# Kernel optimization log

Hardware: AMD Instinct MI355X
Metric: run time of the kernel (lower is better)

Reference implementation:

```python
import jax, jax.numpy as jnp
import numpy as np

HEAD = 64

PARAM_NAMES = ['x_r','x_w','x_k','x_v','x_a','x_g','w0','w1','w2','a0','a1','a2',
               'v0','v1','v2','g1','g2','k_k','k_a','r_k','W_r','W_k','W_v','W_o',
               'ln_x_w','ln_x_b','ln1_w','ln1_b','ln2_w','ln2_b','c_x_k','W_ck','W_cv']


def token_shift(x):
    # previous token, zero-padded at t=0 (stateless shift state)
    return jnp.pad(x, ((0, 0), (1, 0), (0, 0)))[:, :-1]


def layer_norm(x, w, b, eps=1e-5):
    m = jnp.mean(x, -1, keepdims=True)
    v = jnp.mean(jnp.square(x - m), -1, keepdims=True)
    return (x - m) * jax.lax.rsqrt(v + eps) * w + b


def group_norm_heads(x, w, b, H, eps=64e-5):
    # GroupNorm(H, C) as used by RWKV7 ln_x (eps = head_size * 1e-5)
    B, T, C = x.shape
    xh = x.reshape(B, T, H, C // H)
    m = jnp.mean(xh, -1, keepdims=True)
    v = jnp.mean(jnp.square(xh - m), -1, keepdims=True)
    xh = (xh - m) * jax.lax.rsqrt(v + eps)
    return xh.reshape(B, T, C) * w + b


def wkv7(r, w, k, v, a, b):
    # r,w,k,v,a,b: [B,T,H,N]; w is per-channel decay in (0,1)
    # S_t = S_{t-1} * diag(w_t) + (S_{t-1} @ a_t) b_t^T + v_t k_t^T ; y_t = S_t @ r_t
    B, T, H, N = r.shape
    def step(S, inp):
        r_t, w_t, k_t, v_t, a_t, b_t = inp
        sa = jnp.einsum('bhij,bhj->bhi', S, a_t)
        S = S * w_t[:, :, None, :] + sa[..., None] * b_t[:, :, None, :] + v_t[..., None] * k_t[:, :, None, :]
        y = jnp.einsum('bhij,bhj->bhi', S, r_t)
        return S, y
    xs = tuple(jnp.moveaxis(t, 1, 0) for t in (r, w, k, v, a, b))
    S0 = jnp.zeros((B, H, N, N), r.dtype)
    _, ys = jax.lax.scan(step, S0, xs)
    return jnp.moveaxis(ys, 0, 1)


def time_mix(x, v_first, p, is_first_layer):
    B, T, C = x.shape
    H, N = C // HEAD, HEAD
    xx = token_shift(x) - x
    xr = x + xx * p['x_r']; xw = x + xx * p['x_w']; xk = x + xx * p['x_k']
    xv = x + xx * p['x_v']; xa = x + xx * p['x_a']; xg = x + xx * p['x_g']
    r = xr @ p['W_r']
    w = -jax.nn.softplus(-(p['w0'] + jnp.tanh(xw @ p['w1']) @ p['w2'])) - 0.5
    k = xk @ p['W_k']
    v = xv @ p['W_v']
    if is_first_layer:
        v_first = v
    else:
        v = v + (v_first - v) * jax.nn.sigmoid(p['v0'] + (xv @ p['v1']) @ p['v2'])
    a = jax.nn.sigmoid(p['a0'] + (xa @ p['a1']) @ p['a2'])  # in-context learning rate
    g = jax.nn.sigmoid(xg @ p['g1']) @ p['g2']
    kk = (k * p['k_k']).reshape(B, T, H, N)
    kk = kk / jnp.maximum(jnp.linalg.norm(kk, axis=-1, keepdims=True), 1e-12)
    k = k * (1.0 + (a - 1.0) * p['k_a'])
    decay = jnp.exp(-jnp.exp(w)).reshape(B, T, H, N)
    rh = r.reshape(B, T, H, N)
    kh = k.reshape(B, T, H, N)
    vh = v.reshape(B, T, H, N)
    ah = a.reshape(B, T, H, N)
    y = wkv7(rh, decay, kh, vh, -kk, kk * ah).reshape(B, T, C)
    y = group_norm_heads(y, p['ln_x_w'], p['ln_x_b'], H)
    bonus = jnp.sum(rh * kh * p['r_k'], -1, keepdims=True) * vh
    y = y + bonus.reshape(B, T, C)
    return (y * g) @ p['W_o'], v_first


def channel_mix(x, p):
    xx = token_shift(x) - x
    k = x + xx * p['c_x_k']
    k = jnp.square(jax.nn.relu(k @ p['W_ck']))
    return k @ p['W_cv']


def encoder_forward(x, params):
    L = params['W_r'].shape[0]
    v_first = None
    for i in range(L):
        p = {n: params[n][i] for n in PARAM_NAMES}
        att, v_first = time_mix(layer_norm(x, p['ln1_w'], p['ln1_b']), v_first, p, i == 0)
        x = x + att
        x = x + channel_mix(layer_norm(x, p['ln2_w'], p['ln2_b']), p)
    return x


def setup_inputs() -> dict:
    key = jax.random.key(0)
    L, B, T, C = 6, 2, 512, 768
    H, N = C // HEAD, HEAD
    Dw, Da, Dv, Dg, F = 64, 64, 32, 128, 4 * C
    keys = iter(jax.random.split(key, 48))
    def rn(shape, s):
        return jax.random.normal(next(keys), shape, jnp.float32) * s
    def ru(shape):
        return jax.random.uniform(next(keys), shape, jnp.float32)
    inp = {
        'x': rn((B, T, C), 1.0),
        'x_r': ru((L, C)), 'x_w': ru((L, C)), 'x_k': ru((L, C)),
        'x_v': ru((L, C)), 'x_a': ru((L, C)), 'x_g': ru((L, C)),
        'w0': rn((L, C), 0.3), 'w1': rn((L, C, Dw), 0.02), 'w2': rn((L, Dw, C), 0.02),
        'a0': rn((L, C), 0.1), 'a1': rn((L, C, Da), 0.02), 'a2': rn((L, Da, C), 0.02),
        'v0': rn((L, C), 0.1), 'v1': rn((L, C, Dv), 0.02), 'v2': rn((L, Dv, C), 0.02),
        'g1': rn((L, C, Dg), 0.02), 'g2': rn((L, Dg, C), 0.02),
        'k_k': 0.85 + rn((L, C), 0.05), 'k_a': 1.0 + rn((L, C), 0.05),
        'r_k': rn((L, H, N), 0.1),
        'W_r': rn((L, C, C), 0.02), 'W_k': rn((L, C, C), 0.02),
        'W_v': rn((L, C, C), 0.02), 'W_o': rn((L, C, C), 0.02),
        'ln_x_w': 1.0 + rn((L, C), 0.05), 'ln_x_b': rn((L, C), 0.05),
        'ln1_w': 1.0 + rn((L, C), 0.05), 'ln1_b': rn((L, C), 0.05),
        'ln2_w': 1.0 + rn((L, C), 0.05), 'ln2_b': rn((L, C), 0.05),
        'c_x_k': ru((L, C)),
        'W_ck': rn((L, C, F), 0.02), 'W_cv': rn((L, F, C), 0.02),
    }
    return inp


def reference(x, x_r, x_w, x_k, x_v, x_a, x_g, w0, w1, w2, a0, a1, a2, v0, v1, v2,
              g1, g2, k_k, k_a, r_k, W_r, W_k, W_v, W_o, ln_x_w, ln_x_b,
              ln1_w, ln1_b, ln2_w, ln2_b, c_x_k, W_ck, W_cv):
    params = dict(zip(PARAM_NAMES, (x_r, x_w, x_k, x_v, x_a, x_g, w0, w1, w2, a0, a1, a2,
                                    v0, v1, v2, g1, g2, k_k, k_a, r_k, W_r, W_k, W_v, W_o,
                                    ln_x_w, ln_x_b, ln1_w, ln1_b, ln2_w, ln2_b, c_x_k, W_ck, W_cv)))
    return encoder_forward(x, params)
```

## Files before the change

kernel.cpp:

```cpp
#include <hip/hip_runtime.h>
#include <hip/hip_bf16.h>
#include <math.h>

#define LAYERS 6
#define BBATCH 2
#define TT 512
#define CC 768
#define HH 12
#define MT (BBATCH*TT)
#define FF (4*CC)
#define LCH 32
#define NC (TT/LCH)
#define BH (BBATCH*HH)
#define SPAD 65

typedef __hip_bfloat16 bf16;
typedef __bf16 bf16x8 __attribute__((ext_vector_type(8)));
typedef __bf16 bf16x4 __attribute__((ext_vector_type(4)));
typedef float f32x4 __attribute__((ext_vector_type(4)));

__device__ inline bf16 f2b(float f) { return __float2bfloat16(f); }
__device__ inline __bf16 f2bb(float f) {
    __hip_bfloat16 h = __float2bfloat16(f);
    return __builtin_bit_cast(__bf16, h);
}
__device__ inline float bb2f(__bf16 h) {
    return __bfloat162float(__builtin_bit_cast(__hip_bfloat16, h));
}


__global__ __launch_bounds__(256) void copy_f(float* __restrict__ dst, const float* __restrict__ src) {
    size_t i = (size_t)blockIdx.x * 256 + threadIdx.x;
    dst[i] = src[i];
}


__global__ __launch_bounds__(256) void ln_shift_kernel(const float* __restrict__ x,
                                                       const float* __restrict__ w,
                                                       const float* __restrict__ b,
                                                       bf16* __restrict__ out) {
    int row = blockIdx.x;
    int t = row % TT;
    const float* xr = x + (size_t)row * CC;
    const float* xp = xr - CC;
    int tid = threadIdx.x;
    float c0 = xr[tid], c1 = xr[tid + 256], c2 = xr[tid + 512];
    float p0 = 0.f, p1 = 0.f, p2 = 0.f;
    if (t > 0) { p0 = xp[tid]; p1 = xp[tid + 256]; p2 = xp[tid + 512]; }
    float s  = c0 + c1 + c2, q  = c0 * c0 + c1 * c1 + c2 * c2;
    float sp = p0 + p1 + p2, qp = p0 * p0 + p1 * p1 + p2 * p2;
    for (int m = 1; m < 64; m <<= 1) {
        s += __shfl_xor(s, m); q += __shfl_xor(q, m);
        sp += __shfl_xor(sp, m); qp += __shfl_xor(qp, m);
    }
    __shared__ float rs[4], rq[4], rsp[4], rqp[4];
    int wid = tid >> 6;
    if ((tid & 63) == 0) { rs[wid] = s; rq[wid] = q; rsp[wid] = sp; rqp[wid] = qp; }
    __syncthreads();
    s  = rs[0] + rs[1] + rs[2] + rs[3];   q  = rq[0] + rq[1] + rq[2] + rq[3];
    sp = rsp[0] + rsp[1] + rsp[2] + rsp[3]; qp = rqp[0] + rqp[1] + rqp[2] + rqp[3];
    float meanC = s * (1.f / CC);
    float invC  = rsqrtf(q * (1.f / CC) - meanC * meanC + 1e-5f);
    float meanP = sp * (1.f / CC);
    float invP  = rsqrtf(qp * (1.f / CC) - meanP * meanP + 1e-5f);
    bf16* orow = out + (size_t)row * 1536;
    float cv[3] = {c0, c1, c2};
    float pv[3] = {p0, p1, p2};
#pragma unroll
    for (int j = 0; j < 3; ++j) {
        int cc = tid + j * 256;
        float lnc = (cv[j] - meanC) * invC * w[cc] + b[cc];
        float lnp = (t > 0) ? (pv[j] - meanP) * invP * w[cc] + b[cc] : 0.f;
        orow[cc] = f2b(lnc);
        orow[768 + cc] = f2b(lnp - lnc);
    }
}


struct CEntry { const float* W; const float* mix; bf16* dst; int Ksrc, Nsrc, Npad, Kdst, bstart; };
struct CArgs { CEntry e[14]; };

__global__ __launch_bounds__(256) void convert_weights(CArgs ca) {
    int bid = blockIdx.x;
    int idx = 0;
#pragma unroll
    for (int i = 1; i < 14; ++i) if (bid >= ca.e[i].bstart) idx = i;
    CEntry E = ca.e[idx];
    int t = bid - E.bstart;
    int ntN = E.Npad >> 5;
    int tn = (t % ntN) * 32, tk = (t / ntN) * 32;
    __shared__ float tile[32][33];
    int c = threadIdx.x & 31, r0 = threadIdx.x >> 5;
    int ks = tk;
    const float* mixp = nullptr;
    if (tk >= E.Ksrc) { ks = tk - E.Ksrc; mixp = E.mix; }
#pragma unroll
    for (int i = 0; i < 4; ++i) {
        int r = r0 + i * 8;
        float v = (tn + c < E.Nsrc) ? E.W[(size_t)(ks + r) * E.Nsrc + tn + c] : 0.f;
        if (mixp) v *= mixp[ks + r];
        tile[r][c] = v;
    }
    __syncthreads();
#pragma unroll
    for (int i = 0; i < 4; ++i) {
        int r = r0 + i * 8;
        E.dst[(size_t)(tn + r) * E.Kdst + tk + c] = f2b(tile[c][r]);
    }
}


struct EpiG {
    float* outF; bf16* outH;
    const float* p1; const float* p2;
    int epi, ld, ntrue;
};
struct EpiArgs { EpiG g[7]; int nb[8]; };

__device__ inline void epi_store(const EpiG& E, size_t idx, int lc, float v) {
    switch (E.epi) {
        case 0: E.outF[idx] = v; break;
        case 1: E.outH[idx] = f2b(v); break;
        case 2: E.outH[idx] = f2b(tanhf(v)); break;
        case 3: E.outH[idx] = f2b(1.f / (1.f + expf(-v))); break;
        case 4: { float t = fmaxf(v, 0.f); E.outH[idx] = f2b(t * t); } break;
        case 5: E.outF[idx] += v; break;
        case 6: { float z = E.p1[lc] + v; float nz = -z;
                  float sp = (nz > 20.f) ? nz : log1pf(expf(nz));
                  E.outF[idx] = expf(-expf(-sp - 0.5f)); } break;
        case 7: E.outF[idx] = 1.f / (1.f + expf(-(E.p1[lc] + v))); break;
        case 8: { float vv = E.outF[idx];
                  float s = 1.f / (1.f + expf(-(E.p1[lc] + v)));
                  E.outF[idx] = vv + (E.p2[idx] - vv) * s; } break;
    }
}


template<int BM, int BN>
__global__ __launch_bounds__(256) void gemm_multi(const __bf16* __restrict__ A,
                                                  const __bf16* __restrict__ Bt,
                                                  int K, EpiArgs ea) {
    constexpr int FM = BM / 32, FN = BN / 32;
    constexpr int ABYTES = BM * 128;
    constexpr int TOT = (BM + BN) * 128;
    constexpr int NCHUNK = TOT / 4096;
    __shared__ __align__(16) char smem[2][TOT];
    int tid = threadIdx.x;
    int lane = tid & 63, wid = tid >> 6;
    int nwg = gridDim.x * gridDim.y;
    int orig = blockIdx.y * gridDim.x + blockIdx.x;
    int qq = nwg >> 3, rr = nwg & 7, xc = orig & 7, oo = orig >> 3;
    int swz = (xc < rr ? xc * (qq + 1) : rr * (qq + 1) + (xc - rr) * qq) + oo;
    int bn = (swz % gridDim.x) * BN, bm = (swz / gridDim.x) * BM;
    int wm = (wid >> 1) * (BM / 2), wn = (wid & 1) * (BN / 2);
    f32x4 acc[FM][FN];
#pragma unroll
    for (int i = 0; i < FM; ++i)
#pragma unroll
        for (int j = 0; j < FN; ++j) acc[i][j] = (f32x4){0.f, 0.f, 0.f, 0.f};

    int nk = K >> 6;
    auto stage = [&](int buf, int k0) {
        char* sb = &smem[buf][0];
#pragma unroll
        for (int c = 0; c < NCHUNK; ++c) {
            int d = c * 4096 + tid * 16;
            int isB = d >= ABYTES;
            int dd = isB ? d - ABYTES : d;
            int row = dd >> 7;
            int slot = (dd >> 4) & 7;
            int su = slot ^ (row & 7);
            const __bf16* src = isB ? (Bt + (size_t)(bn + row) * K + k0 + su * 8)
                                    : (A  + (size_t)(bm + row) * K + k0 + su * 8);
            char* ldst = sb + c * 4096 + (tid & 192) * 16;
            __builtin_amdgcn_global_load_lds(
                (const __attribute__((address_space(1))) unsigned int*)src,
                (__attribute__((address_space(3))) unsigned int*)ldst, 16, 0, 0);
        }
    };

    stage(0, 0);
    __syncthreads();
    for (int t = 0; t < nk; ++t) {
        if (t + 1 < nk) stage((t + 1) & 1, (t + 1) * 64);
        const char* sA = &smem[t & 1][0];
        const char* sB = &smem[t & 1][ABYTES];
        int u = lane >> 4, r0 = lane & 15;
        bf16x8 af[2][FM], bfr[2][FN];
#pragma unroll
        for (int ks = 0; ks < 2; ++ks) {
#pragma unroll
            for (int i = 0; i < FM; ++i) {
                int row = wm + i * 16 + r0;
                int slot = (ks * 4 + u) ^ (row & 7);
                af[ks][i] = *(const bf16x8*)(sA + row * 128 + slot * 16);
            }
#pragma unroll
            for (int j = 0; j < FN; ++j) {
                int row = wn + j * 16 + r0;
                int slot = (ks * 4 + u) ^ (row & 7);
                bfr[ks][j] = *(const bf16x8*)(sB + row * 128 + slot * 16);
            }
        }
#pragma unroll
        for (int ks = 0; ks < 2; ++ks)
#pragma unroll
            for (int i = 0; i < FM; ++i)
#pragma unroll
                for (int j = 0; j < FN; ++j)
                    acc[i][j] = __builtin_amdgcn_mfma_f32_16x16x32_bf16(af[ks][i], bfr[ks][j], acc[i][j], 0, 0, 0);
        __syncthreads();
    }

    int gid = 0;
#pragma unroll 1
    while (bn >= ea.nb[gid + 1]) ++gid;
    EpiG E = ea.g[gid];
    int colBase = ea.nb[gid];
#pragma unroll
    for (int i = 0; i < FM; ++i) {
#pragma unroll
        for (int j = 0; j < FN; ++j) {
#pragma unroll
            for (int q = 0; q < 4; ++q) {
                int gm = bm + wm + i * 16 + (lane >> 4) * 4 + q;
                int lc = bn + wn + j * 16 + (lane & 15) - colBase;
                if (lc < E.ntrue)
                    epi_store(E, (size_t)gm * E.ld + lc, lc, acc[i][j][q]);
            }
        }
    }
}


struct G2G { const __bf16* A; const __bf16* Bt; float* outF; const float* p1; const float* p2; int K; int epi; };
struct G2Args { G2G g[4]; };

template<int BM, int BN>
__global__ __launch_bounds__(256) void gemm_g2(G2Args ga) {
    G2G G = ga.g[blockIdx.z];
    const __bf16* A = G.A;
    const __bf16* Bt = G.Bt;
    int K = G.K;
    constexpr int FM = BM / 32, FN = BN / 32;
    constexpr int ABYTES = BM * 64;
    constexpr int TOT = (BM + BN) * 64;
    constexpr int NCHUNK = TOT / 4096;
    __shared__ __align__(16) char smem[2][TOT];
    int tid = threadIdx.x;
    int lane = tid & 63, wid = tid >> 6;
    int bm = blockIdx.y * BM, bn = blockIdx.x * BN;
    int wm = (wid >> 1) * (BM / 2), wn = (wid & 1) * (BN / 2);
    f32x4 acc[FM][FN];
#pragma unroll
    for (int i = 0; i < FM; ++i)
#pragma unroll
        for (int j = 0; j < FN; ++j) acc[i][j] = (f32x4){0.f, 0.f, 0.f, 0.f};

    int nk = K >> 5;
    auto stage = [&](int buf, int k0) {
        char* sb = &smem[buf][0];
#pragma unroll
        for (int c = 0; c < NCHUNK; ++c) {
            int d = c * 4096 + tid * 16;
            int isB = d >= ABYTES;
            int dd = isB ? d - ABYTES : d;
            int row = dd >> 6;
            int u = (dd >> 4) & 3;
            int su = u ^ ((row >> 1) & 3);
            const __bf16* src = isB ? (Bt + (size_t)(bn + row) * K + k0 + su * 8)
                                    : (A  + (size_t)(bm + row) * K + k0 + su * 8);
            char* ldst = sb + c * 4096 + (tid & 192) * 16;
            __builtin_amdgcn_global_load_lds(
                (const __attribute__((address_space(1))) unsigned int*)src,
                (__attribute__((address_space(3))) unsigned int*)ldst, 16, 0, 0);
        }
    };

    stage(0, 0);
    __syncthreads();
    for (int t = 0; t < nk; ++t) {
        if (t + 1 < nk) stage((t + 1) & 1, (t + 1) * 32);
        const char* sA = &smem[t & 1][0];
        const char* sB = &smem[t & 1][ABYTES];
        int u = lane >> 4, r0 = lane & 15;
        bf16x8 af[FM], bfr[FN];
#pragma unroll
        for (int i = 0; i < FM; ++i) {
            int row = wm + i * 16 + r0;
            int su = u ^ ((row >> 1) & 3);
            af[i] = *(const bf16x8*)(sA + row * 64 + su * 16);
        }
#pragma unroll
        for (int j = 0; j < FN; ++j) {
            int row = wn + j * 16 + r0;
            int su = u ^ ((row >> 1) & 3);
            bfr[j] = *(const bf16x8*)(sB + row * 64 + su * 16);
        }
#pragma unroll
        for (int i = 0; i < FM; ++i)
#pragma unroll
            for (int j = 0; j < FN; ++j)
                acc[i][j] = __builtin_amdgcn_mfma_f32_16x16x32_bf16(af[i], bfr[j], acc[i][j], 0, 0, 0);
        __syncthreads();
    }

    EpiG E;
    E.outF = G.outF; E.outH = nullptr; E.p1 = G.p1; E.p2 = G.p2;
    E.epi = G.epi; E.ld = 768; E.ntrue = 768;
#pragma unroll
    for (int i = 0; i < FM; ++i) {
#pragma unroll
        for (int j = 0; j < FN; ++j) {
#pragma unroll
            for (int q = 0; q < 4; ++q) {
                int gm = bm + wm + i * 16 + (lane >> 4) * 4 + q;
                int lc = bn + wn + j * 16 + (lane & 15);
                epi_store(E, (size_t)gm * 768 + lc, lc, acc[i][j][q]);
            }
        }
    }
}


__global__ __launch_bounds__(256) void chunkA_kernel(
    const float* __restrict__ r, const float* __restrict__ wd,
    const float* __restrict__ kraw, const float* __restrict__ av_,
    const float* __restrict__ v,
    const float* __restrict__ kkw, const float* __restrict__ kaw,
    float* __restrict__ kupd,
    float* __restrict__ yintra, float* __restrict__ zrO,
    __bf16* __restrict__ mtHi, __bf16* __restrict__ mtLo,
    float* __restrict__ zcO) {
    int c = blockIdx.x, bh = blockIdx.y;
    int b = bh / HH, h = bh % HH;
    __shared__ float Di[LCH][SPAD];
    __shared__ float Ah[LCH][SPAD];
    __shared__ float Bh[LCH][SPAD];
    __shared__ float Kh[LCH][SPAD];
    __shared__ float Rh[LCH][SPAD];
    __shared__ float Vt[LCH][SPAD];
    __shared__ float Qm[LCH][SPAD];
    __shared__ float Gba[LCH][LCH], Gka[LCH][LCH], Grb[LCH][LCH], Grk[LCH][LCH];
    int tid = threadIdx.x;
    int n = tid & 63, tq = tid >> 6;
    size_t base = ((size_t)(b * TT + c * LCH)) * CC + h * 64 + n;
    int cvec = h * 64 + n;
    float kkwv = kkw[cvec], kawv = kaw[cvec];
#pragma unroll
    for (int e = 0; e < 8; ++e) {
        int t = tq * 8 + e;
        size_t off = base + (size_t)t * CC;
        float kr = kraw[off];
        float aval = av_[off];
        float kk0 = kr * kkwv;
        float ss = kk0 * kk0;
        for (int m = 1; m < 64; m <<= 1) ss += __shfl_xor(ss, m);
        float rinv = 1.f / fmaxf(sqrtf(ss), 1e-12f);
        float kkv = kk0 * rinv;
        float ku = kr * (1.f + (aval - 1.f) * kawv);
        kupd[off] = ku;
        Di[t][n] = wd[off];
        Ah[t][n] = -kkv;
        Bh[t][n] = kkv * aval;
        Kh[t][n] = ku;
        Rh[t][n] = r[off];
        Vt[t][n] = v[off];
    }
    __syncthreads();
    if (tid < 64) {
        float d = 1.f;
        for (int t = 0; t < LCH; ++t) { d *= Di[t][tid]; Di[t][tid] = d; }
    }
    __syncthreads();
#pragma unroll
    for (int e = 0; e < 8; ++e) {
        int t = tq * 8 + e;
        float di = Di[t][n];
        float dp = (t == 0) ? 1.f : Di[t - 1][n];
        float inv = 1.f / di;
        Ah[t][n] *= dp;
        Bh[t][n] *= inv;
        Kh[t][n] *= inv;
        Rh[t][n] *= di;
    }
    __syncthreads();
    {
        int tp = tid >> 4, sp = tid & 15;
        int t0 = 2 * tp, s0 = 2 * sp;
        float gba00 = 0.f, gba01 = 0.f, gba10 = 0.f, gba11 = 0.f;
        float gka00 = 0.f, gka01 = 0.f, gka10 = 0.f, gka11 = 0.f;
        float grb00 = 0.f, grb01 = 0.f, grb10 = 0.f, grb11 = 0.f;
        float grk00 = 0.f, grk01 = 0.f, grk10 = 0.f, grk11 = 0.f;
#pragma unroll 4
        for (int j = 0; j < 64; ++j) {
            float a0 = Ah[t0][j], a1 = Ah[t0 + 1][j];
            float r0 = Rh[t0][j], r1 = Rh[t0 + 1][j];
            float b0 = Bh[s0][j], b1 = Bh[s0 + 1][j];
            float k0 = Kh[s0][j], k1 = Kh[s0 + 1][j];
            gba00 = fmaf(a0, b0, gba00); gba01 = fmaf(a0, b1, gba01);
            gba10 = fmaf(a1, b0, gba10); gba11 = fmaf(a1, b1, gba11);
            gka00 = fmaf(a0, k0, gka00); gka01 = fmaf(a0, k1, gka01);
            gka10 = fmaf(a1, k0, gka10); gka11 = fmaf(a1, k1, gka11);
            grb00 = fmaf(r0, b0, grb00); grb01 = fmaf(r0, b1, grb01);
            grb10 = fmaf(r1, b0, grb10); grb11 = fmaf(r1, b1, grb11);
            grk00 = fmaf(r0, k0, grk00); grk01 = fmaf(r0, k1, grk01);
            grk10 = fmaf(r1, k0, grk10); grk11 = fmaf(r1, k1, grk11);
        }
#pragma unroll
        for (int dt = 0; dt < 2; ++dt) {
            int t = t0 + dt;
#pragma unroll
            for (int ds = 0; ds < 2; ++ds) {
                int s = s0 + ds;
                float vba = dt ? (ds ? gba11 : gba10) : (ds ? gba01 : gba00);
                float vka = dt ? (ds ? gka11 : gka10) : (ds ? gka01 : gka00);
                float vrb = dt ? (ds ? grb11 : grb10) : (ds ? grb01 : grb00);
                float vrk = dt ? (ds ? grk11 : grk10) : (ds ? grk01 : grk00);
                Gba[t][s] = (s < t)  ? vba : 0.f;
                Gka[t][s] = (s < t)  ? vka : 0.f;
                Grb[t][s] = (s <= t) ? vrb : 0.f;
                Grk[t][s] = (s <= t) ? vrk : 0.f;
            }
        }
    }
    __syncthreads();
    {
        float acc[8];
#pragma unroll
        for (int e = 0; e < 8; ++e) acc[e] = 0.f;
        for (int s = 0; s < LCH; ++s) {
            float vs = Vt[s][n];
#pragma unroll
            for (int e = 0; e < 8; ++e)
                acc[e] = fmaf(Gka[tq * 8 + e][s], vs, acc[e]);
        }
#pragma unroll
        for (int e = 0; e < 8; ++e) Qm[tq * 8 + e][n] = acc[e];
    }
    __syncthreads();
    if (tq == 0) {
        for (int t = 1; t < LCH; ++t) {
            float acc = Ah[t][n];
            for (int s = 0; s < t; ++s) acc = fmaf(Gba[t][s], Ah[s][n], acc);
            Ah[t][n] = acc;
        }
    } else if (tq == 1) {
        for (int t = 1; t < LCH; ++t) {
            float acc = Qm[t][n];
            for (int s = 0; s < t; ++s) acc = fmaf(Gba[t][s], Qm[s][n], acc);
            Qm[t][n] = acc;
        }
    }
    __syncthreads();
    size_t obase = ((size_t)(bh * NC + c)) * LCH * 64;
    {
        float accY[8], accZ[8];
#pragma unroll
        for (int e = 0; e < 8; ++e) { accY[e] = 0.f; accZ[e] = Rh[tq * 8 + e][n]; }
        for (int s = 0; s < LCH; ++s) {
            float vs = Vt[s][n], qs = Qm[s][n], us = Ah[s][n];
#pragma unroll
            for (int e = 0; e < 8; ++e) {
                int t = tq * 8 + e;
                float grk_ = Grk[t][s], grb_ = Grb[t][s];
                accY[e] = fmaf(grk_, vs, fmaf(grb_, qs, accY[e]));
                accZ[e] = fmaf(grb_, us, accZ[e]);
            }
        }
#pragma unroll
        for (int e = 0; e < 8; ++e) {
            int t = tq * 8 + e;
            yintra[obase + t * 64 + n] = accY[e];
            zrO[obase + t * 64 + n] = accZ[e];
        }
    }
    {
        int pi = tid >> 4, ni = tid & 15;
        float accM[4][4], accZc[4][4];
#pragma unroll
        for (int dp = 0; dp < 4; ++dp)
#pragma unroll
            for (int dn = 0; dn < 4; ++dn) { accM[dp][dn] = 0.f; accZc[dp][dn] = 0.f; }
        for (int s = 0; s < LCH; ++s) {
            float aa[4], vv[4], qq[4], bb[4], kk[4];
#pragma unroll
            for (int d = 0; d < 4; ++d) {
                aa[d] = Ah[s][4 * pi + d];
                vv[d] = Vt[s][4 * pi + d];
                qq[d] = Qm[s][4 * pi + d];
                bb[d] = Bh[s][4 * ni + d];
                kk[d] = Kh[s][4 * ni + d];
            }
#pragma unroll
            for (int dp = 0; dp < 4; ++dp)
#pragma unroll
                for (int dn = 0; dn < 4; ++dn) {
                    accM[dp][dn]  = fmaf(aa[dp], bb[dn], accM[dp][dn]);
                    accZc[dp][dn] = fmaf(vv[dp], kk[dn], fmaf(qq[dp], bb[dn], accZc[dp][dn]));
                }
        }
        size_t mbase = ((size_t)(bh * NC + c)) * 4096;
        float dl[4];
#pragma unroll
        for (int dn = 0; dn < 4; ++dn) dl[dn] = Di[LCH - 1][4 * ni + dn];
#pragma unroll
        for (int dp = 0; dp < 4; ++dp) {
            int p = 4 * pi + dp;
            f32x4 z4;
#pragma unroll
            for (int dn = 0; dn < 4; ++dn) z4[dn] = dl[dn] * accZc[dp][dn];
            *(f32x4*)(zcO + mbase + p * 64 + 4 * ni) = z4;
        }
#pragma unroll
        for (int dn = 0; dn < 4; ++dn) {
            int nn = 4 * ni + dn;
            float dlv = dl[dn];
            bf16x4 h4, l4;
#pragma unroll
            for (int dp = 0; dp < 4; ++dp) {
                int p = 4 * pi + dp;
                float mm = (accM[dp][dn] + ((p == nn) ? 1.f : 0.f)) * dlv;
                __bf16 hb = f2bb(mm);
                h4[dp] = hb;
                l4[dp] = f2bb(mm - bb2f(hb));
            }
            *(bf16x4*)(mtHi + mbase + (size_t)nn * 64 + 4 * pi) = h4;
            *(bf16x4*)(mtLo + mbase + (size_t)nn * 64 + 4 * pi) = l4;
        }
    }
}


__global__ __launch_bounds__(256) void chunkB1_kernel(
    const float* __restrict__ zc,
    const __bf16* __restrict__ mtHi,
    const __bf16* __restrict__ mtLo,
    float* __restrict__ schk) {
    int bh = blockIdx.x;
    int tid = threadIdx.x;
    int lane = tid & 63, w = tid >> 6;
    int r0 = lane & 15, u = lane >> 4;
    __shared__ __align__(16) float S[64][68];
    for (int i = tid; i < 64 * 68; i += 256) (&S[0][0])[i] = 0.f;
    const float* zbase = zc + (size_t)bh * NC * 4096;
    const __bf16* hbase = mtHi + (size_t)bh * NC * 4096;
    const __bf16* lbase = mtLo + (size_t)bh * NC * 4096;
    float* sbase = schk + (size_t)bh * NC * 4096;
    int arow = w * 16 + r0;

    bf16x8 mh[2][4][2], ml[2][4][2];
    f32x4 zf[2][4];
#pragma unroll
    for (int ct = 0; ct < 4; ++ct) {
#pragma unroll
        for (int ks = 0; ks < 2; ++ks) {
            size_t mo = (size_t)(ct * 16 + r0) * 64 + ks * 32 + u * 8;
            mh[0][ct][ks] = *(const bf16x8*)(hbase + mo);
            ml[0][ct][ks] = *(const bf16x8*)(lbase + mo);
        }
#pragma unroll
        for (int q = 0; q < 4; ++q)
            zf[0][ct][q] = zbase[(size_t)(w * 16 + u * 4 + q) * 64 + ct * 16 + r0];
    }
    __syncthreads();
#pragma unroll
    for (int c = 0; c < NC - 1; ++c) {
        const int cb = c & 1;
        if (c + 1 < NC - 1) {
            const __bf16* hn = hbase + (size_t)(c + 1) * 4096;
            const __bf16* ln = lbase + (size_t)(c + 1) * 4096;
            const float* zn = zbase + (size_t)(c + 1) * 4096;
#pragma unroll
            for (int ct = 0; ct < 4; ++ct) {
#pragma unroll
                for (int ks = 0; ks < 2; ++ks) {
                    size_t mo = (size_t)(ct * 16 + r0) * 64 + ks * 32 + u * 8;
                    mh[cb ^ 1][ct][ks] = *(const bf16x8*)(hn + mo);
                    ml[cb ^ 1][ct][ks] = *(const bf16x8*)(ln + mo);
                }
#pragma unroll
                for (int q = 0; q < 4; ++q)
                    zf[cb ^ 1][ct][q] = zn[(size_t)(w * 16 + u * 4 + q) * 64 + ct * 16 + r0];
            }
        }
        bf16x8 ah[2], al[2];
#pragma unroll
        for (int ks = 0; ks < 2; ++ks) {
            f32x4 s0 = *(const f32x4*)&S[arow][ks * 32 + u * 8];
            f32x4 s1 = *(const f32x4*)&S[arow][ks * 32 + u * 8 + 4];
#pragma unroll
            for (int e = 0; e < 4; ++e) {
                __bf16 h0 = f2bb(s0[e]);
                ah[ks][e] = h0;
                al[ks][e] = f2bb(s0[e] - bb2f(h0));
                __bf16 h1 = f2bb(s1[e]);
                ah[ks][4 + e] = h1;
                al[ks][4 + e] = f2bb(s1[e] - bb2f(h1));
            }
        }
        f32x4 acc[4];
#pragma unroll
        for (int ct = 0; ct < 4; ++ct) {
            acc[ct] = zf[cb][ct];
#pragma unroll
            for (int ks = 0; ks < 2; ++ks) {
                acc[ct] = __builtin_amdgcn_mfma_f32_16x16x32_bf16(ah[ks], mh[cb][ct][ks], acc[ct], 0, 0, 0);
                acc[ct] = __builtin_amdgcn_mfma_f32_16x16x32_bf16(ah[ks], ml[cb][ct][ks], acc[ct], 0, 0, 0);
                acc[ct] = __builtin_amdgcn_mfma_f32_16x16x32_bf16(al[ks], mh[cb][ct][ks], acc[ct], 0, 0, 0);
            }
        }
        __syncthreads();
        float* cp = sbase + (size_t)(c + 1) * 4096;
#pragma unroll
        for (int ct = 0; ct < 4; ++ct) {
#pragma unroll
            for (int q = 0; q < 4; ++q) {
                int row = w * 16 + u * 4 + q;
                int col = ct * 16 + r0;
                S[row][col] = acc[ct][q];
                cp[(size_t)row * 64 + col] = acc[ct][q];
            }
        }
        __syncthreads();
    }
}


__global__ __launch_bounds__(256) void chunkY_kernel(
    const float* __restrict__ yintra, const float* __restrict__ zrI,
    const float* __restrict__ schk,
    const float* __restrict__ r, const float* __restrict__ kupd,
    const float* __restrict__ v, const float* __restrict__ g,
    const float* __restrict__ rk, const float* __restrict__ lw,
    const float* __restrict__ lb, bf16* __restrict__ out) {
    int c = blockIdx.x, bh = blockIdx.y;
    int b = bh / HH, h = bh % HH;
    __shared__ float Y[LCH][SPAD];
    __shared__ float Zr[LCH][SPAD];
    __shared__ float Sh[64][SPAD];
    int tid = threadIdx.x;
    int n = tid & 63, tq = tid >> 6;
    size_t obase = ((size_t)(bh * NC + c)) * LCH * 64;
#pragma unroll
    for (int e = 0; e < 8; ++e) {
        int idx = tid + e * 256;
        int row = idx >> 6, col = idx & 63;
        Y[row][col] = yintra[obase + idx];
        Zr[row][col] = zrI[obase + idx];
    }
    if (c > 0) {
        size_t sbase = ((size_t)(bh * NC + c)) * 4096;
#pragma unroll
        for (int e = 0; e < 16; ++e) {
            int idx = tid + e * 256;
            Sh[idx >> 6][idx & 63] = schk[sbase + idx];
        }
    }
    __syncthreads();
    if (c > 0) {
        float acc[8];
#pragma unroll
        for (int e = 0; e < 8; ++e) acc[e] = 0.f;
        for (int p = 0; p < 64; ++p) {
            float sv = Sh[n][p];
#pragma unroll
            for (int e = 0; e < 8; ++e)
                acc[e] = fmaf(Zr[tq * 8 + e][p], sv, acc[e]);
        }
#pragma unroll
        for (int e = 0; e < 8; ++e) Y[tq * 8 + e][n] += acc[e];
    }
    size_t rowbase = ((size_t)(b * TT + c * LCH)) * CC + h * 64 + n;
    float rkv = rk[h * 64 + n];
    float lwv = lw[h * 64 + n], lbv = lb[h * 64 + n];
#pragma unroll
    for (int e = 0; e < 8; ++e) {
        int t = tq * 8 + e;
        size_t off = rowbase + (size_t)t * CC;
        float yv = Y[t][n];
        float rv = r[off], kv = kupd[off], vv = v[off];
        float s1 = yv, s2 = yv * yv, s3 = rv * kv * rkv;
        for (int m = 1; m < 64; m <<= 1) {
            s1 += __shfl_xor(s1, m);
            s2 += __shfl_xor(s2, m);
            s3 += __shfl_xor(s3, m);
        }
        float mean = s1 * (1.f / 64.f);
        float var  = s2 * (1.f / 64.f) - mean * mean;
        float inv  = rsqrtf(var + 64e-5f);
        float val  = (yv - mean) * inv * lwv + lbv + s3 * vv;
        out[off] = f2b(val * g[off]);
    }
}


extern "C" void kernel_launch(void* const* d_in, const int* in_sizes, int n_in,
                              void* d_out, int out_size, void* d_ws, size_t ws_size,
                              hipStream_t stream) {
    (void)in_sizes; (void)n_in; (void)out_size;
    const float* x    = (const float*)d_in[0];
    const float* x_r  = (const float*)d_in[1];
    const float* x_w  = (const float*)d_in[2];
    const float* x_k  = (const float*)d_in[3];
    const float* x_v  = (const float*)d_in[4];
    const float* x_a  = (const float*)d_in[5];
    const float* x_g  = (const float*)d_in[6];
    const float* w0   = (const float*)d_in[7];
    const float* w1   = (const float*)d_in[8];
    const float* w2   = (const float*)d_in[9];
    const float* a0   = (const float*)d_in[10];
    const float* a1   = (const float*)d_in[11];
    const float* a2   = (const float*)d_in[12];
    const float* v0   = (const float*)d_in[13];
    const float* v1   = (const float*)d_in[14];
    const float* v2   = (const float*)d_in[15];
    const float* g1   = (const float*)d_in[16];
    const float* g2   = (const float*)d_in[17];
    const float* k_k  = (const float*)d_in[18];
    const float* k_a  = (const float*)d_in[19];
    const float* r_k  = (const float*)d_in[20];
    const float* W_r  = (const float*)d_in[21];
    const float* W_k  = (const float*)d_in[22];
    const float* W_v  = (const float*)d_in[23];
    const float* W_o  = (const float*)d_in[24];
    const float* ln_x_w = (const float*)d_in[25];
    const float* ln_x_b = (const float*)d_in[26];
    const float* ln1_w  = (const float*)d_in[27];
    const float* ln1_b  = (const float*)d_in[28];
    const float* ln2_w  = (const float*)d_in[29];
    const float* ln2_b  = (const float*)d_in[30];
    const float* c_x_k  = (const float*)d_in[31];
    const float* W_ck   = (const float*)d_in[32];
    const float* W_cv   = (const float*)d_in[33];

    const size_t MC = (size_t)MT * CC;
    char* wsb = (char*)d_ws;
    size_t woff = 0;
    auto alloc = [&](size_t bytes) -> void* {
        void* p = wsb + woff;
        woff += (bytes + 255) & ~(size_t)255;
        return p;
    };
    bf16* Bcat  = (bf16*)alloc((size_t)2624 * 1536 * 2);
    bf16* Bck   = (bf16*)alloc((size_t)3072 * 1536 * 2);
    bf16* w2t   = (bf16*)alloc((size_t)768 * 64 * 2);
    bf16* a2t   = (bf16*)alloc((size_t)768 * 64 * 2);
    bf16* v2t   = (bf16*)alloc((size_t)768 * 32 * 2);
    bf16* g2t   = (bf16*)alloc((size_t)768 * 128 * 2);
    bf16* Wo_t  = (bf16*)alloc((size_t)768 * 768 * 2);
    bf16* Wcv_t = (bf16*)alloc((size_t)768 * 3072 * 2);
    bf16* A1    = (bf16*)alloc((size_t)MT * 1536 * 2);
    float* rbuf  = (float*)alloc(MC * 4);
    float* kraw  = (float*)alloc(MC * 4);
    float* kupd  = (float*)alloc(MC * 4);
    float* vbuf  = (float*)alloc(MC * 4);
    float* vfirst= (float*)alloc(MC * 4);
    float* abuf  = (float*)alloc(MC * 4);
    float* dbuf  = (float*)alloc(MC * 4);
    float* gbuf  = (float*)alloc(MC * 4);
    bf16* w1o   = (bf16*)alloc((size_t)MT * 64 * 2);
    bf16* a1o   = (bf16*)alloc((size_t)MT * 64 * 2);
    bf16* v1o   = (bf16*)alloc((size_t)MT * 32 * 2);
    bf16* g1o   = (bf16*)alloc((size_t)MT * 128 * 2);
    bf16* hbuf  = (bf16*)alloc((size_t)MT * FF * 2);
    bf16* ghout = (bf16*)alloc(MC * 2);
    float* yintraW = (float*)alloc((size_t)BH * NC * LCH * 64 * 4);
    float* zrW     = (float*)alloc((size_t)BH * NC * LCH * 64 * 4);
    __bf16* mtHiW  = (__bf16*)alloc((size_t)BH * NC * 4096 * 2);
    __bf16* mtLoW  = (__bf16*)alloc((size_t)BH * NC * 4096 * 2);
    float* zcW     = (float*)alloc((size_t)BH * NC * 4096 * 4);
    float* schkW   = (float*)alloc((size_t)BH * NC * 4096 * 4);
    if (woff > ws_size) return;

    float* xcur = (float*)d_out;
    copy_f<<<MC / 256, 256, 0, stream>>>(xcur, x);

    for (int l = 0; l < LAYERS; ++l) {
        size_t oC = (size_t)l * CC;
        float* vptr = (l == 0) ? vfirst : vbuf;

        CArgs ca;
        ca.e[0]  = {W_r  + (size_t)l * 589824, x_r + oC, Bcat,               768, 768, 768, 1536, 0};
        ca.e[1]  = {W_k  + (size_t)l * 589824, x_k + oC, Bcat + (size_t)768  * 1536, 768, 768, 768, 1536, 0};
        ca.e[2]  = {W_v  + (size_t)l * 589824, x_v + oC, Bcat + (size_t)1536 * 1536, 768, 768, 768, 1536, 0};
        ca.e[3]  = {w1   + (size_t)l * 49152,  x_w + oC, Bcat + (size_t)2304 * 1536, 768, 64, 64, 1536, 0};
        ca.e[4]  = {a1   + (size_t)l * 49152,  x_a + oC, Bcat + (size_t)2368 * 1536, 768, 64, 64, 1536, 0};
        ca.e[5]  = {g1   + (size_t)l * 98304,  x_g + oC, Bcat + (size_t)2432 * 1536, 768, 128, 128, 1536, 0};
        ca.e[6]  = {v1   + (size_t)l * 24576,  x_v + oC, Bcat + (size_t)2560 * 1536, 768, 32, 64, 1536, 0};
        ca.e[7]  = {W_ck + (size_t)l * 2359296, c_x_k + oC, Bck, 768, 3072, 3072, 1536, 0};
        ca.e[8]  = {w2   + (size_t)l * 49152,  nullptr, w2t,   64, 768, 768, 64, 0};
        ca.e[9]  = {a2   + (size_t)l * 49152,  nullptr, a2t,   64, 768, 768, 64, 0};
        ca.e[10] = {v2   + (size_t)l * 24576,  nullptr, v2t,   32, 768, 768, 32, 0};
        ca.e[11] = {g2   + (size_t)l * 98304,  nullptr, g2t,  128, 768, 768, 128, 0};
        ca.e[12] = {W_o  + (size_t)l * 589824, nullptr, Wo_t, 768, 768, 768, 768, 0};
        ca.e[13] = {W_cv + (size_t)l * 2359296, nullptr, Wcv_t, 3072, 768, 768, 3072, 0};
        int btot = 0;
        for (int i = 0; i < 14; ++i) {
            ca.e[i].bstart = btot;
            btot += (ca.e[i].Npad >> 5) * (ca.e[i].Kdst >> 5);
        }
        convert_weights<<<btot, 256, 0, stream>>>(ca);

        ln_shift_kernel<<<MT, 256, 0, stream>>>(xcur, ln1_w + oC, ln1_b + oC, A1);

        EpiArgs e1;
        e1.g[0] = {rbuf,  nullptr, nullptr, nullptr, 0, 768, 768};
        e1.g[1] = {kraw,  nullptr, nullptr, nullptr, 0, 768, 768};
        e1.g[2] = {vptr,  nullptr, nullptr, nullptr, 0, 768, 768};
        e1.g[3] = {nullptr, w1o, nullptr, nullptr, 2, 64, 64};
        e1.g[4] = {nullptr, a1o, nullptr, nullptr, 1, 64, 64};
        e1.g[5] = {nullptr, g1o, nullptr, nullptr, 3, 128, 128};
        e1.g[6] = {nullptr, v1o, nullptr, nullptr, 1, 32, 32};
        int nb1[8] = {0, 768, 1536, 2304, 2368, 2432, 2560, 2624};
        for (int i = 0; i < 8; ++i) e1.nb[i] = nb1[i];
        gemm_multi<128, 64><<<dim3(41, 8), 256, 0, stream>>>((const __bf16*)A1, (const __bf16*)Bcat, 1536, e1);

        G2Args g2a;
        g2a.g[0] = {(const __bf16*)w1o, (const __bf16*)w2t, dbuf, w0 + oC, nullptr, 64, 6};
        g2a.g[1] = {(const __bf16*)a1o, (const __bf16*)a2t, abuf, a0 + oC, nullptr, 64, 7};
        g2a.g[2] = {(const __bf16*)g1o, (const __bf16*)g2t, gbuf, nullptr, nullptr, 128, 0};
        g2a.g[3] = {(const __bf16*)v1o, (const __bf16*)v2t, vbuf, v0 + oC, vfirst, 32, 8};
        gemm_g2<128, 64><<<dim3(12, 8, (l == 0) ? 3 : 4), 256, 0, stream>>>(g2a);

        chunkA_kernel<<<dim3(NC, BH), 256, 0, stream>>>(rbuf, dbuf, kraw, abuf, vptr,
                                                        k_k + oC, k_a + oC, kupd,
                                                        yintraW, zrW, mtHiW, mtLoW, zcW);
        chunkB1_kernel<<<BH, 256, 0, stream>>>(zcW, mtHiW, mtLoW, schkW);
        chunkY_kernel<<<dim3(NC, BH), 256, 0, stream>>>(yintraW, zrW, schkW,
                                                        rbuf, kupd, vptr, gbuf,
                                                        r_k + (size_t)l * 768,
                                                        ln_x_w + oC, ln_x_b + oC, ghout);

        EpiArgs eo;
        eo.g[0] = {xcur, nullptr, nullptr, nullptr, 5, 768, 768};
        eo.nb[0] = 0; for (int i = 1; i < 8; ++i) eo.nb[i] = 1 << 30;
        eo.nb[1] = 768;
        gemm_multi<64, 64><<<dim3(12, 16), 256, 0, stream>>>((const __bf16*)ghout, (const __bf16*)Wo_t, 768, eo);

        ln_shift_kernel<<<MT, 256, 0, stream>>>(xcur, ln2_w + oC, ln2_b + oC, A1);

        EpiArgs ec;
        ec.g[0] = {nullptr, hbuf, nullptr, nullptr, 4, 3072, 3072};
        ec.nb[0] = 0; for (int i = 1; i < 8; ++i) ec.nb[i] = 1 << 30;
        ec.nb[1] = 3072;
        gemm_multi<128, 64><<<dim3(48, 8), 256, 0, stream>>>((const __bf16*)A1, (const __bf16*)Bck, 1536, ec);

        EpiArgs ev;
        ev.g[0] = {xcur, nullptr, nullptr, nullptr, 5, 768, 768};
        ev.nb[0] = 0; for (int i = 1; i < 8; ++i) ev.nb[i] = 1 << 30;
        ev.nb[1] = 768;
        gemm_multi<64, 64><<<dim3(12, 16), 256, 0, stream>>>((const __bf16*)hbuf, (const __bf16*)Wcv_t, 3072, ev);
    }
}
```

Baseline: 1.410 ms.

## Convert all layer weights in one batched launch and shrink GEMM M-tiles

Weight transpose/convert to bf16 for all six layers now runs in a single launch with a layer grid dimension, writing into per-layer workspace buffers instead of a reused scratch buffer per layer. This removes five kernel launches and lets the conversion run as one large, well-occupied grid instead of serialising with each layer's compute. The first projection and FFN-up GEMMs also switch from 128-row to 64-row tiles with twice the grid rows, for more blocks across the CUs at the cost of less reuse per block. Workspace use grows by roughly six times the converted-weight footprint.

```diff
diff --git a/kernel.cpp b/kernel.cpp
--- a/kernel.cpp
+++ b/kernel.cpp
@@ -77,15 +77,19 @@
 }
 
 
-struct CEntry { const float* W; const float* mix; bf16* dst; int Ksrc, Nsrc, Npad, Kdst, bstart; };
+struct CEntry { const float* W; const float* mix; bf16* dst;
+                int Ksrc, Nsrc, Npad, Kdst, bstart, wstr, dstr; };
 struct CArgs { CEntry e[14]; };
 
 __global__ __launch_bounds__(256) void convert_weights(CArgs ca) {
     int bid = blockIdx.x;
+    int l = blockIdx.y;
     int idx = 0;
 #pragma unroll
     for (int i = 1; i < 14; ++i) if (bid >= ca.e[i].bstart) idx = i;
     CEntry E = ca.e[idx];
+    const float* Wsrc = E.W + (size_t)l * E.wstr;
+    bf16* d = E.dst + (size_t)l * E.dstr;
     int t = bid - E.bstart;
     int ntN = E.Npad >> 5;
     int tn = (t % ntN) * 32, tk = (t / ntN) * 32;
@@ -93,11 +97,11 @@
     int c = threadIdx.x & 31, r0 = threadIdx.x >> 5;
     int ks = tk;
     const float* mixp = nullptr;
-    if (tk >= E.Ksrc) { ks = tk - E.Ksrc; mixp = E.mix; }
+    if (tk >= E.Ksrc) { ks = tk - E.Ksrc; mixp = E.mix + (size_t)l * CC; }
 #pragma unroll
     for (int i = 0; i < 4; ++i) {
         int r = r0 + i * 8;
-        float v = (tn + c < E.Nsrc) ? E.W[(size_t)(ks + r) * E.Nsrc + tn + c] : 0.f;
+        float v = (tn + c < E.Nsrc) ? Wsrc[(size_t)(ks + r) * E.Nsrc + tn + c] : 0.f;
         if (mixp) v *= mixp[ks + r];
         tile[r][c] = v;
     }
@@ -105,7 +109,7 @@
 #pragma unroll
     for (int i = 0; i < 4; ++i) {
         int r = r0 + i * 8;
-        E.dst[(size_t)(tn + r) * E.Kdst + tk + c] = f2b(tile[c][r]);
+        d[(size_t)(tn + r) * E.Kdst + tk + c] = f2b(tile[c][r]);
     }
 }
 
@@ -742,14 +746,22 @@
         woff += (bytes + 255) & ~(size_t)255;
         return p;
     };
-    bf16* Bcat  = (bf16*)alloc((size_t)2624 * 1536 * 2);
-    bf16* Bck   = (bf16*)alloc((size_t)3072 * 1536 * 2);
-    bf16* w2t   = (bf16*)alloc((size_t)768 * 64 * 2);
-    bf16* a2t   = (bf16*)alloc((size_t)768 * 64 * 2);
-    bf16* v2t   = (bf16*)alloc((size_t)768 * 32 * 2);
-    bf16* g2t   = (bf16*)alloc((size_t)768 * 128 * 2);
-    bf16* Wo_t  = (bf16*)alloc((size_t)768 * 768 * 2);
-    bf16* Wcv_t = (bf16*)alloc((size_t)768 * 3072 * 2);
+    const size_t S_Bcat = (size_t)2624 * 1536;
+    const size_t S_Bck  = (size_t)3072 * 1536;
+    const size_t S_w2t  = (size_t)768 * 64;
+    const size_t S_a2t  = (size_t)768 * 64;
+    const size_t S_v2t  = (size_t)768 * 32;
+    const size_t S_g2t  = (size_t)768 * 128;
+    const size_t S_Wo   = (size_t)768 * 768;
+    const size_t S_Wcv  = (size_t)768 * 3072;
+    bf16* BcatA = (bf16*)alloc(S_Bcat * LAYERS * 2);
+    bf16* BckA  = (bf16*)alloc(S_Bck  * LAYERS * 2);
+    bf16* w2tA  = (bf16*)alloc(S_w2t  * LAYERS * 2);
+    bf16* a2tA  = (bf16*)alloc(S_a2t  * LAYERS * 2);
+    bf16* v2tA  = (bf16*)alloc(S_v2t  * LAYERS * 2);
+    bf16* g2tA  = (bf16*)alloc(S_g2t  * LAYERS * 2);
+    bf16* WoA   = (bf16*)alloc(S_Wo   * LAYERS * 2);
+    bf16* WcvA  = (bf16*)alloc(S_Wcv  * LAYERS * 2);
     bf16* A1    = (bf16*)alloc((size_t)MT * 1536 * 2);
     float* rbuf  = (float*)alloc(MC * 4);
     float* kraw  = (float*)alloc(MC * 4);
@@ -776,31 +788,39 @@
     float* xcur = (float*)d_out;
     copy_f<<<MC / 256, 256, 0, stream>>>(xcur, x);
 
+    CArgs ca;
+    ca.e[0]  = {W_r,  x_r,  BcatA,                    768, 768, 768, 1536, 0, 589824, (int)S_Bcat};
+    ca.e[1]  = {W_k,  x_k,  BcatA + (size_t)768  * 1536, 768, 768, 768, 1536, 0, 589824, (int)S_Bcat};
+    ca.e[2]  = {W_v,  x_v,  BcatA + (size_t)1536 * 1536, 768, 768, 768, 1536, 0, 589824, (int)S_Bcat};
+    ca.e[3]  = {w1,   x_w,  BcatA + (size_t)2304 * 1536, 768, 64, 64, 1536, 0, 49152, (int)S_Bcat};
+    ca.e[4]  = {a1,   x_a,  BcatA + (size_t)2368 * 1536, 768, 64, 64, 1536, 0, 49152, (int)S_Bcat};
+    ca.e[5]  = {g1,   x_g,  BcatA + (size_t)2432 * 1536, 768, 128, 128, 1536, 0, 98304, (int)S_Bcat};
+    ca.e[6]  = {v1,   x_v,  BcatA + (size_t)2560 * 1536, 768, 32, 64, 1536, 0, 24576, (int)S_Bcat};
+    ca.e[7]  = {W_ck, c_x_k, BckA, 768, 3072, 3072, 1536, 0, 2359296, (int)S_Bck};
+    ca.e[8]  = {w2,   nullptr, w2tA,   64, 768, 768, 64, 0, 49152, (int)S_w2t};
+    ca.e[9]  = {a2,   nullptr, a2tA,   64, 768, 768, 64, 0, 49152, (int)S_a2t};
+    ca.e[10] = {v2,   nullptr, v2tA,   32, 768, 768, 32, 0, 24576, (int)S_v2t};
+    ca.e[11] = {g2,   nullptr, g2tA,  128, 768, 768, 128, 0, 98304, (int)S_g2t};
+    ca.e[12] = {W_o,  nullptr, WoA,  768, 768, 768, 768, 0, 589824, (int)S_Wo};
+    ca.e[13] = {W_cv, nullptr, WcvA, 3072, 768, 768, 3072, 0, 2359296, (int)S_Wcv};
+    int btot = 0;
+    for (int i = 0; i < 14; ++i) {
+        ca.e[i].bstart = btot;
+        btot += (ca.e[i].Npad >> 5) * (ca.e[i].Kdst >> 5);
+    }
+    convert_weights<<<dim3(btot, LAYERS), 256, 0, stream>>>(ca);
+
     for (int l = 0; l < LAYERS; ++l) {
         size_t oC = (size_t)l * CC;
         float* vptr = (l == 0) ? vfirst : vbuf;
-
-        CArgs ca;
-        ca.e[0]  = {W_r  + (size_t)l * 589824, x_r + oC, Bcat,               768, 768, 768, 1536, 0};
-        ca.e[1]  = {W_k  + (size_t)l * 589824, x_k + oC, Bcat + (size_t)768  * 1536, 768, 768, 768, 1536, 0};
-        ca.e[2]  = {W_v  + (size_t)l * 589824, x_v + oC, Bcat + (size_t)1536 * 1536, 768, 768, 768, 1536, 0};
-        ca.e[3]  = {w1   + (size_t)l * 49152,  x_w + oC, Bcat + (size_t)2304 * 1536, 768, 64, 64, 1536, 0};
-        ca.e[4]  = {a1   + (size_t)l * 49152,  x_a + oC, Bcat + (size_t)2368 * 1536, 768, 64, 64, 1536, 0};
-        ca.e[5]  = {g1   + (size_t)l * 98304,  x_g + oC, Bcat + (size_t)2432 * 1536, 768, 128, 128, 1536, 0};
-        ca.e[6]  = {v1   + (size_t)l * 24576,  x_v + oC, Bcat + (size_t)2560 * 1536, 768, 32, 64, 1536, 0};
-        ca.e[7]  = {W_ck + (size_t)l * 2359296, c_x_k + oC, Bck, 768, 3072, 3072, 1536, 0};
-        ca.e[8]  = {w2   + (size_t)l * 49152,  nullptr, w2t,   64, 768, 768, 64, 0};
-        ca.e[9]  = {a2   + (size_t)l * 49152,  nullptr, a2t,   64, 768, 768, 64, 0};
-        ca.e[10] = {v2   + (size_t)l * 24576,  nullptr, v2t,   32, 768, 768, 32, 0};
-        ca.e[11] = {g2   + (size_t)l * 98304,  nullptr, g2t,  128, 768, 768, 128, 0};
-        ca.e[12] = {W_o  + (size_t)l * 589824, nullptr, Wo_t, 768, 768, 768, 768, 0};
-        ca.e[13] = {W_cv + (size_t)l * 2359296, nullptr, Wcv_t, 3072, 768, 768, 3072, 0};
-        int btot = 0;
-        for (int i = 0; i < 14; ++i) {
-            ca.e[i].bstart = btot;
-            btot += (ca.e[i].Npad >> 5) * (ca.e[i].Kdst >> 5);
-        }
-        convert_weights<<<btot, 256, 0, stream>>>(ca);
+        const __bf16* Bcat  = (const __bf16*)(BcatA + (size_t)l * S_Bcat);
+        const __bf16* Bck   = (const __bf16*)(BckA  + (size_t)l * S_Bck);
+        const __bf16* w2t   = (const __bf16*)(w2tA  + (size_t)l * S_w2t);
+        const __bf16* a2t   = (const __bf16*)(a2tA  + (size_t)l * S_a2t);
+        const __bf16* v2t   = (const __bf16*)(v2tA  + (size_t)l * S_v2t);
+        const __bf16* g2t   = (const __bf16*)(g2tA  + (size_t)l * S_g2t);
+        const __bf16* Wo_t  = (const __bf16*)(WoA   + (size_t)l * S_Wo);
+        const __bf16* Wcv_t = (const __bf16*)(WcvA  + (size_t)l * S_Wcv);
 
         ln_shift_kernel<<<MT, 256, 0, stream>>>(xcur, ln1_w + oC, ln1_b + oC, A1);
 
@@ -814,13 +834,13 @@
         e1.g[6] = {nullptr, v1o, nullptr, nullptr, 1, 32, 32};
         int nb1[8] = {0, 768, 1536, 2304, 2368, 2432, 2560, 2624};
         for (int i = 0; i < 8; ++i) e1.nb[i] = nb1[i];
-        gemm_multi<128, 64><<<dim3(41, 8), 256, 0, stream>>>((const __bf16*)A1, (const __bf16*)Bcat, 1536, e1);
+        gemm_multi<64, 64><<<dim3(41, 16), 256, 0, stream>>>((const __bf16*)A1, Bcat, 1536, e1);
 
         G2Args g2a;
-        g2a.g[0] = {(const __bf16*)w1o, (const __bf16*)w2t, dbuf, w0 + oC, nullptr, 64, 6};
-        g2a.g[1] = {(const __bf16*)a1o, (const __bf16*)a2t, abuf, a0 + oC, nullptr, 64, 7};
-        g2a.g[2] = {(const __bf16*)g1o, (const __bf16*)g2t, gbuf, nullptr, nullptr, 128, 0};
-        g2a.g[3] = {(const __bf16*)v1o, (const __bf16*)v2t, vbuf, v0 + oC, vfirst, 32, 8};
+        g2a.g[0] = {(const __bf16*)w1o, w2t, dbuf, w0 + oC, nullptr, 64, 6};
+        g2a.g[1] = {(const __bf16*)a1o, a2t, abuf, a0 + oC, nullptr, 64, 7};
+        g2a.g[2] = {(const __bf16*)g1o, g2t, gbuf, nullptr, nullptr, 128, 0};
+        g2a.g[3] = {(const __bf16*)v1o, v2t, vbuf, v0 + oC, vfirst, 32, 8};
         gemm_g2<128, 64><<<dim3(12, 8, (l == 0) ? 3 : 4), 256, 0, stream>>>(g2a);
 
         chunkA_kernel<<<dim3(NC, BH), 256, 0, stream>>>(rbuf, dbuf, kraw, abuf, vptr,
@@ -836,7 +856,7 @@
         eo.g[0] = {xcur, nullptr, nullptr, nullptr, 5, 768, 768};
         eo.nb[0] = 0; for (int i = 1; i < 8; ++i) eo.nb[i] = 1 << 30;
         eo.nb[1] = 768;
-        gemm_multi<64, 64><<<dim3(12, 16), 256, 0, stream>>>((const __bf16*)ghout, (const __bf16*)Wo_t, 768, eo);
+        gemm_multi<64, 64><<<dim3(12, 16), 256, 0, stream>>>((const __bf16*)ghout, Wo_t, 768, eo);
 
         ln_shift_kernel<<<MT, 256, 0, stream>>>(xcur, ln2_w + oC, ln2_b + oC, A1);
 
@@ -844,12 +864,12 @@
         ec.g[0] = {nullptr, hbuf, nullptr, nullptr, 4, 3072, 3072};
         ec.nb[0] = 0; for (int i = 1; i < 8; ++i) ec.nb[i] = 1 << 30;
         ec.nb[1] = 3072;
-        gemm_multi<128, 64><<<dim3(48, 8), 256, 0, stream>>>((const __bf16*)A1, (const __bf16*)Bck, 1536, ec);
+        gemm_multi<64, 64><<<dim3(48, 16), 256, 0, stream>>>((const __bf16*)A1, Bck, 1536, ec);
 
         EpiArgs ev;
         ev.g[0] = {xcur, nullptr, nullptr, nullptr, 5, 768, 768};
         ev.nb[0] = 0; for (int i = 1; i < 8; ++i) ev.nb[i] = 1 << 30;
         ev.nb[1] = 768;
-        gemm_multi<64, 64><<<dim3(12, 16), 256, 0, stream>>>((const __bf16*)hbuf, (const __bf16*)Wcv_t, 3072, ev);
-    }
-}
+        gemm_multi<64, 64><<<dim3(12, 16), 256, 0, stream>>>((const __bf16*)hbuf, Wcv_t, 3072, ev);
+    }
+}
```

After: 1.356 ms. -3.8%, faster.
